# Performance work log

Hardware: AMD Instinct MI355X
Metric: run time of the kernel (lower is better)

Reference implementation:

```python
import jax, jax.numpy as jnp
import numpy as np

S = 64   # state_dim
C = 27   # children per internal node


def setup_inputs() -> dict:
    key = jax.random.key(0)
    ks = jax.random.split(key, 16)
    def f(k, shp, scale=0.02):
        return jax.random.normal(k, shp, dtype=jnp.float32) * scale
    return {
        "external_input": f(ks[0], (S, 5), 1.0),
        "state0":  f(ks[1], (S, 5), 0.01),          # root state buffer
        "states1": f(ks[2], (C, S, 5), 0.01),        # 27 level-1 node states
        "states2": f(ks[3], (C, C, S, 5), 0.01),     # 729 leaf states, grouped by parent
        "agg_W0":  f(ks[4], (S * 5, S * 5 * C)),     # root child_aggregator
        "agg_b0":  f(ks[5], (S * 5,)),
        "agg_W1":  f(ks[6], (C, S * 5, S * 5 * C)),  # batched level-1 aggregators
        "agg_b1":  f(ks[7], (C, S * 5)),
        "up_W1_0": f(ks[8], (64, S * 10)),           # root update_net layer 1
        "up_b1_0": f(ks[9], (64,)),
        "up_W2_0": f(ks[10], (S * 5, 64)),           # root update_net layer 2
        "up_b2_0": f(ks[11], (S * 5,)),
        "up_W1_1": f(ks[12], (C, 64, S * 10)),       # batched level-1 update_nets
        "up_b1_1": f(ks[13], (C, 64)),
        "up_W2_1": f(ks[14], (C, S * 5, 64)),
        "up_b2_1": f(ks[15], (C, S * 5)),
    }


def reference(external_input, state0, states1, states2,
              agg_W0, agg_b0, agg_W1, agg_b1,
              up_W1_0, up_b1_0, up_W2_0, up_b2_0,
              up_W1_1, up_b1_1, up_W2_1, up_b2_1):
    # --- level 2 (leaves): forward just returns their state ---
    leaf_flat = states2.reshape(C, C * S * 5)  # per level-1 parent: stacked+flattened children

    # --- level 1: all 27 nodes processed as one batched GEMV ---
    agg1 = jnp.einsum('nij,nj->ni', agg_W1, leaf_flat) + agg_b1        # [27, S*5]
    comb1 = jnp.concatenate([states1.reshape(C, S * 5), agg1], axis=-1)  # [27, S*10]
    h1 = jax.nn.relu(jnp.einsum('nkj,nj->nk', up_W1_1, comb1) + up_b1_1)  # [27, 64]
    upd1 = jnp.einsum('nij,nj->ni', up_W2_1, h1) + up_b2_1             # [27, S*5]
    new_states1 = states1 + upd1.reshape(C, S, 5)

    # --- root: external input added, then aggregate updated children ---
    s0 = state0 + external_input
    agg0 = agg_W0 @ new_states1.reshape(-1) + agg_b0                   # [S*5]
    comb0 = jnp.concatenate([s0.reshape(-1), agg0])                    # [S*10]
    h0 = jax.nn.relu(up_W1_0 @ comb0 + up_b1_0)
    new_state0 = s0 + (up_W2_0 @ h0 + up_b2_0).reshape(S, 5)
    return new_state0
```

## Files before the change

### kernel.cpp

```cpp
#include <hip/hip_runtime.h>
#include <hip/hip_bf16.h>


__device__ __forceinline__ float wave_reduce_sum(float v) {
    v += __shfl_xor(v, 32, 64);
    v += __shfl_xor(v, 16, 64);
    v += __shfl_xor(v, 8, 64);
    v += __shfl_xor(v, 4, 64);
    v += __shfl_xor(v, 2, 64);
    v += __shfl_xor(v, 1, 64);
    return v;
}

__device__ __forceinline__ float fma4s(float4 w, float4 x, float acc) {
    acc = fmaf(w.x, x.x, acc);
    acc = fmaf(w.y, x.y, acc);
    acc = fmaf(w.z, x.z, acc);
    acc = fmaf(w.w, x.w, acc);
    return acc;
}

__device__ __forceinline__ float4 add4(float4 a, float4 b) {
    return make_float4(a.x + b.x, a.y + b.y, a.z + b.z, a.w + b.w);
}

__global__ void __launch_bounds__(256) k1_gemv(
    const float* __restrict__ W,
    const float* __restrict__ x,
    const float* __restrict__ bias,
    float*       __restrict__ y)
{
    const int b    = blockIdx.x;
    const int node = b / 40;
    const int row0 = node * 320 + (b % 40) * 8;
    const int tid  = threadIdx.x;

    const float4* __restrict__ xf = reinterpret_cast<const float4*>(x) + (size_t)node * 2160;
    const float4* wp[8];
    #pragma unroll
    for (int r = 0; r < 8; ++r)
        wp[r] = reinterpret_cast<const float4*>(W) + (size_t)(row0 + r) * 2160;

    float4 acc[8];
    #pragma unroll
    for (int r = 0; r < 8; ++r) acc[r] = make_float4(0.f, 0.f, 0.f, 0.f);

    for (int j = tid; j < 2160; j += 256) {
        float4 xv = xf[j];
        #pragma unroll
        for (int r = 0; r < 8; ++r) {
            float4 w = wp[r][j];
            acc[r].x = fmaf(w.x, xv.x, acc[r].x);
            acc[r].y = fmaf(w.y, xv.y, acc[r].y);
            acc[r].z = fmaf(w.z, xv.z, acc[r].z);
            acc[r].w = fmaf(w.w, xv.w, acc[r].w);
        }
    }

    float s[8];
    #pragma unroll
    for (int r = 0; r < 8; ++r) {
        s[r] = (acc[r].x + acc[r].y) + (acc[r].z + acc[r].w);
        s[r] = wave_reduce_sum(s[r]);
    }

    __shared__ float red[4][8];
    const int wv = tid >> 6, lane = tid & 63;
    if (lane == 0) {
        #pragma unroll
        for (int r = 0; r < 8; ++r) red[wv][r] = s[r];
    }
    __syncthreads();
    if (tid < 8) {
        float v = red[0][tid] + red[1][tid] + red[2][tid] + red[3][tid];
        y[row0 + tid] = v + bias[row0 + tid];
    }
}

__global__ void __launch_bounds__(256) k2a_h(
    const float* __restrict__ states1,
    const float* __restrict__ agg1,
    const float* __restrict__ W1,
    const float* __restrict__ b1,
    float*       __restrict__ h1)
{
    __shared__ float comb[640];
    const int nb  = blockIdx.x;
    const int n   = nb / 16;
    const int tid = threadIdx.x;

    float4* combf = reinterpret_cast<float4*>(comb);
    const float4* __restrict__ s1f = reinterpret_cast<const float4*>(states1) + (size_t)n * 80;
    const float4* __restrict__ a1f = reinterpret_cast<const float4*>(agg1) + (size_t)n * 80;
    if (tid < 80)       combf[tid] = s1f[tid];
    else if (tid < 160) combf[tid] = a1f[tid - 80];
    __syncthreads();

    const int wv = tid >> 6, lane = tid & 63;
    const int k  = (nb % 16) * 4 + wv;
    const float4* __restrict__ Wf = reinterpret_cast<const float4*>(W1) + ((size_t)n * 64 + k) * 160;
    float acc = 0.f;
    #pragma unroll
    for (int j = lane; j < 160; j += 64)
        acc = fma4s(Wf[j], combf[j], acc);
    acc = wave_reduce_sum(acc);
    if (lane == 0) h1[n * 64 + k] = fmaxf(acc + b1[n * 64 + k], 0.f);
}

__global__ void __launch_bounds__(256) k2b_ns(
    const float* __restrict__ states1,
    const float* __restrict__ h1,
    const float* __restrict__ W2,
    const float* __restrict__ b2,
    float*       __restrict__ ns1)
{
    const int tid  = threadIdx.x;
    const int wv   = tid >> 6, lane = tid & 63;
    const int i    = blockIdx.x * 4 + wv;
    const int n    = i / 320;
    float acc = W2[(size_t)i * 64 + lane] * h1[n * 64 + lane];
    acc = wave_reduce_sum(acc);
    if (lane == 0) ns1[i] = states1[i] + acc + b2[i];
}

__global__ void __launch_bounds__(256) k3_gemv(
    const float* __restrict__ W,
    const float* __restrict__ x,
    float*       __restrict__ yp)
{
    const int b   = blockIdx.x;
    const int cs  = b / 80;
    const int r0  = (b % 80) * 4;
    const int tid = threadIdx.x;

    const float4* __restrict__ xf  = reinterpret_cast<const float4*>(x);
    const float4* __restrict__ w0p = reinterpret_cast<const float4*>(W) + (size_t)(r0 + 0) * 2160;
    const float4* __restrict__ w1p = reinterpret_cast<const float4*>(W) + (size_t)(r0 + 1) * 2160;
    const float4* __restrict__ w2p = reinterpret_cast<const float4*>(W) + (size_t)(r0 + 2) * 2160;
    const float4* __restrict__ w3p = reinterpret_cast<const float4*>(W) + (size_t)(r0 + 3) * 2160;

    float4 a0 = make_float4(0.f, 0.f, 0.f, 0.f), a1 = a0, a2 = a0, a3 = a0;
    const int jend = cs * 540 + 540;
    for (int j = cs * 540 + tid; j < jend; j += 256) {
        float4 xv = xf[j];
        float4 w0 = w0p[j];
        float4 w1 = w1p[j];
        float4 w2 = w2p[j];
        float4 w3 = w3p[j];
        a0.x = fmaf(w0.x, xv.x, a0.x); a0.y = fmaf(w0.y, xv.y, a0.y);
        a0.z = fmaf(w0.z, xv.z, a0.z); a0.w = fmaf(w0.w, xv.w, a0.w);
        a1.x = fmaf(w1.x, xv.x, a1.x); a1.y = fmaf(w1.y, xv.y, a1.y);
        a1.z = fmaf(w1.z, xv.z, a1.z); a1.w = fmaf(w1.w, xv.w, a1.w);
        a2.x = fmaf(w2.x, xv.x, a2.x); a2.y = fmaf(w2.y, xv.y, a2.y);
        a2.z = fmaf(w2.z, xv.z, a2.z); a2.w = fmaf(w2.w, xv.w, a2.w);
        a3.x = fmaf(w3.x, xv.x, a3.x); a3.y = fmaf(w3.y, xv.y, a3.y);
        a3.z = fmaf(w3.z, xv.z, a3.z); a3.w = fmaf(w3.w, xv.w, a3.w);
    }
    float s0 = (a0.x + a0.y) + (a0.z + a0.w);
    float s1 = (a1.x + a1.y) + (a1.z + a1.w);
    float s2 = (a2.x + a2.y) + (a2.z + a2.w);
    float s3 = (a3.x + a3.y) + (a3.z + a3.w);
    s0 = wave_reduce_sum(s0);
    s1 = wave_reduce_sum(s1);
    s2 = wave_reduce_sum(s2);
    s3 = wave_reduce_sum(s3);

    __shared__ float red[4][4];
    const int wv = tid >> 6, lane = tid & 63;
    if (lane == 0) { red[wv][0] = s0; red[wv][1] = s1; red[wv][2] = s2; red[wv][3] = s3; }
    __syncthreads();
    if (tid < 4) {
        yp[cs * 320 + r0 + tid] =
            red[0][tid] + red[1][tid] + red[2][tid] + red[3][tid];
    }
}

__global__ void __launch_bounds__(256) k4a_h(
    const float* __restrict__ state0,
    const float* __restrict__ ext,
    const float* __restrict__ agg0p,
    const float* __restrict__ agg_b0,
    const float* __restrict__ W1,
    const float* __restrict__ b1,
    float*       __restrict__ h0)
{
    __shared__ float comb[640];
    const int tid = threadIdx.x;
    float4* combf = reinterpret_cast<float4*>(comb);
    const float4* __restrict__ s0f = reinterpret_cast<const float4*>(state0);
    const float4* __restrict__ exf = reinterpret_cast<const float4*>(ext);
    const float4* __restrict__ p0  = reinterpret_cast<const float4*>(agg0p);
    const float4* __restrict__ p1  = p0 + 80;
    const float4* __restrict__ p2  = p0 + 160;
    const float4* __restrict__ p3  = p0 + 240;
    const float4* __restrict__ b0f = reinterpret_cast<const float4*>(agg_b0);
    if (tid < 80) {
        combf[tid] = add4(s0f[tid], exf[tid]);
    } else if (tid < 160) {
        int jj = tid - 80;
        combf[tid] = add4(add4(add4(p0[jj], p1[jj]), add4(p2[jj], p3[jj])), b0f[jj]);
    }
    __syncthreads();

    const int wv = tid >> 6, lane = tid & 63;
    const int k  = blockIdx.x * 4 + wv;
    const float4* __restrict__ Wf = reinterpret_cast<const float4*>(W1) + (size_t)k * 160;
    float acc = 0.f;
    #pragma unroll
    for (int j = lane; j < 160; j += 64)
        acc = fma4s(Wf[j], combf[j], acc);
    acc = wave_reduce_sum(acc);
    if (lane == 0) h0[k] = fmaxf(acc + b1[k], 0.f);
}

__global__ void __launch_bounds__(256) k4b_out(
    const float* __restrict__ state0,
    const float* __restrict__ ext,
    const float* __restrict__ h0,
    const float* __restrict__ W2,
    const float* __restrict__ b2,
    float*       __restrict__ out)
{
    const int tid  = threadIdx.x;
    const int wv   = tid >> 6, lane = tid & 63;
    const int i    = blockIdx.x * 4 + wv;
    float acc = W2[(size_t)i * 64 + lane] * h0[lane];
    acc = wave_reduce_sum(acc);
    if (lane == 0) out[i] = state0[i] + ext[i] + acc + b2[i];
}

extern "C" void kernel_launch(void* const* d_in, const int* in_sizes, int n_in,
                              void* d_out, int out_size, void* d_ws, size_t ws_size,
                              hipStream_t stream) {
    const float* ext      = (const float*)d_in[0];
    const float* state0   = (const float*)d_in[1];
    const float* states1  = (const float*)d_in[2];
    const float* states2  = (const float*)d_in[3];
    const float* agg_W0   = (const float*)d_in[4];
    const float* agg_b0   = (const float*)d_in[5];
    const float* agg_W1   = (const float*)d_in[6];
    const float* agg_b1   = (const float*)d_in[7];
    const float* up_W1_0  = (const float*)d_in[8];
    const float* up_b1_0  = (const float*)d_in[9];
    const float* up_W2_0  = (const float*)d_in[10];
    const float* up_b2_0  = (const float*)d_in[11];
    const float* up_W1_1  = (const float*)d_in[12];
    const float* up_b1_1  = (const float*)d_in[13];
    const float* up_W2_1  = (const float*)d_in[14];
    const float* up_b2_1  = (const float*)d_in[15];

    float* out   = (float*)d_out;
    float* ws    = (float*)d_ws;
    float* agg1  = ws;
    float* h1    = ws + 8640;
    float* ns1   = ws + 10368;
    float* agg0p = ws + 19008;
    float* h0    = ws + 20288;

    k1_gemv<<<1080, 256, 0, stream>>>(agg_W1, states2, agg_b1, agg1);
    k2a_h  <<<432,  256, 0, stream>>>(states1, agg1, up_W1_1, up_b1_1, h1);
    k2b_ns <<<2160, 256, 0, stream>>>(states1, h1, up_W2_1, up_b2_1, ns1);
    k3_gemv<<<320,  256, 0, stream>>>(agg_W0, ns1, agg0p);
    k4a_h  <<<16,   256, 0, stream>>>(state0, ext, agg0p, agg_b0, up_W1_0, up_b1_0, h0);
    k4b_out<<<80,   256, 0, stream>>>(state0, ext, h0, up_W2_0, up_b2_0, out);
}
```

Baseline: 71.12 us.

## Fuse per-node update MLP layers into single kernels for level-1 and root

Merges the two-layer update MLP kernels (hidden layer and output layer) into one kernel each for the level-1 nodes and the root, keeping the hidden activations in shared memory. This removes two kernel launches and the global round trips for h1/h0. In exchange, level-1 work now runs on only 27 blocks and the root on a single block, so far fewer CUs pull the roughly 2.2 MB of level-1 update weights.

```diff
diff --git a/kernel.cpp b/kernel.cpp
--- a/kernel.cpp
+++ b/kernel.cpp
@@ -77,17 +77,20 @@
     }
 }
 
-__global__ void __launch_bounds__(256) k2a_h(
+__global__ void __launch_bounds__(512) k2_mlp(
     const float* __restrict__ states1,
     const float* __restrict__ agg1,
     const float* __restrict__ W1,
     const float* __restrict__ b1,
-    float*       __restrict__ h1)
-{
-    __shared__ float comb[640];
-    const int nb  = blockIdx.x;
-    const int n   = nb / 16;
+    const float* __restrict__ W2,
+    const float* __restrict__ b2,
+    float*       __restrict__ ns1)
+{
+    __shared__ __align__(16) float comb[640];
+    __shared__ float h[64];
+    const int n   = blockIdx.x;
     const int tid = threadIdx.x;
+    const int wv  = tid >> 6, lane = tid & 63;
 
     float4* combf = reinterpret_cast<float4*>(comb);
     const float4* __restrict__ s1f = reinterpret_cast<const float4*>(states1) + (size_t)n * 80;
@@ -96,31 +99,33 @@
     else if (tid < 160) combf[tid] = a1f[tid - 80];
     __syncthreads();
 
-    const int wv = tid >> 6, lane = tid & 63;
-    const int k  = (nb % 16) * 4 + wv;
-    const float4* __restrict__ Wf = reinterpret_cast<const float4*>(W1) + ((size_t)n * 64 + k) * 160;
-    float acc = 0.f;
-    #pragma unroll
-    for (int j = lane; j < 160; j += 64)
-        acc = fma4s(Wf[j], combf[j], acc);
-    acc = wave_reduce_sum(acc);
-    if (lane == 0) h1[n * 64 + k] = fmaxf(acc + b1[n * 64 + k], 0.f);
-}
-
-__global__ void __launch_bounds__(256) k2b_ns(
-    const float* __restrict__ states1,
-    const float* __restrict__ h1,
-    const float* __restrict__ W2,
-    const float* __restrict__ b2,
-    float*       __restrict__ ns1)
-{
-    const int tid  = threadIdx.x;
-    const int wv   = tid >> 6, lane = tid & 63;
-    const int i    = blockIdx.x * 4 + wv;
-    const int n    = i / 320;
-    float acc = W2[(size_t)i * 64 + lane] * h1[n * 64 + lane];
-    acc = wave_reduce_sum(acc);
-    if (lane == 0) ns1[i] = states1[i] + acc + b2[i];
+    const float4* __restrict__ cf = reinterpret_cast<const float4*>(comb);
+    #pragma unroll
+    for (int kk = 0; kk < 8; ++kk) {
+        const int k = wv * 8 + kk;
+        const float4* __restrict__ Wf = reinterpret_cast<const float4*>(W1) + ((size_t)n * 64 + k) * 160;
+        float acc = 0.f;
+        #pragma unroll
+        for (int j = lane; j < 160; j += 64)
+            acc = fma4s(Wf[j], cf[j], acc);
+        acc = wave_reduce_sum(acc);
+        if (lane == 0) h[k] = fmaxf(acc + b1[n * 64 + k], 0.f);
+    }
+    __syncthreads();
+
+    if (tid < 320) {
+        const float4* __restrict__ w = reinterpret_cast<const float4*>(W2 + ((size_t)n * 320 + tid) * 64);
+        float acc = 0.f;
+        #pragma unroll
+        for (int j4 = 0; j4 < 16; ++j4) {
+            float4 ww = w[j4];
+            acc = fmaf(ww.x, h[4 * j4 + 0], acc);
+            acc = fmaf(ww.y, h[4 * j4 + 1], acc);
+            acc = fmaf(ww.z, h[4 * j4 + 2], acc);
+            acc = fmaf(ww.w, h[4 * j4 + 3], acc);
+        }
+        ns1[n * 320 + tid] = states1[n * 320 + tid] + acc + b2[n * 320 + tid];
+    }
 }
 
 __global__ void __launch_bounds__(256) k3_gemv(
@@ -175,58 +180,62 @@
     }
 }
 
-__global__ void __launch_bounds__(256) k4a_h(
+__global__ void __launch_bounds__(512) k4_root(
     const float* __restrict__ state0,
     const float* __restrict__ ext,
     const float* __restrict__ agg0p,
-    const float* __restrict__ agg_b0,
+    const float* __restrict__ aggb0,
     const float* __restrict__ W1,
     const float* __restrict__ b1,
-    float*       __restrict__ h0)
-{
-    __shared__ float comb[640];
+    const float* __restrict__ W2,
+    const float* __restrict__ b2,
+    float*       __restrict__ out)
+{
+    __shared__ __align__(16) float comb[640];
+    __shared__ float h[64];
     const int tid = threadIdx.x;
+    const int wv  = tid >> 6, lane = tid & 63;
+
     float4* combf = reinterpret_cast<float4*>(comb);
     const float4* __restrict__ s0f = reinterpret_cast<const float4*>(state0);
     const float4* __restrict__ exf = reinterpret_cast<const float4*>(ext);
     const float4* __restrict__ p0  = reinterpret_cast<const float4*>(agg0p);
-    const float4* __restrict__ p1  = p0 + 80;
-    const float4* __restrict__ p2  = p0 + 160;
-    const float4* __restrict__ p3  = p0 + 240;
-    const float4* __restrict__ b0f = reinterpret_cast<const float4*>(agg_b0);
+    const float4* __restrict__ b0f = reinterpret_cast<const float4*>(aggb0);
     if (tid < 80) {
         combf[tid] = add4(s0f[tid], exf[tid]);
     } else if (tid < 160) {
         int jj = tid - 80;
-        combf[tid] = add4(add4(add4(p0[jj], p1[jj]), add4(p2[jj], p3[jj])), b0f[jj]);
-    }
-    __syncthreads();
-
-    const int wv = tid >> 6, lane = tid & 63;
-    const int k  = blockIdx.x * 4 + wv;
-    const float4* __restrict__ Wf = reinterpret_cast<const float4*>(W1) + (size_t)k * 160;
-    float acc = 0.f;
-    #pragma unroll
-    for (int j = lane; j < 160; j += 64)
-        acc = fma4s(Wf[j], combf[j], acc);
-    acc = wave_reduce_sum(acc);
-    if (lane == 0) h0[k] = fmaxf(acc + b1[k], 0.f);
-}
-
-__global__ void __launch_bounds__(256) k4b_out(
-    const float* __restrict__ state0,
-    const float* __restrict__ ext,
-    const float* __restrict__ h0,
-    const float* __restrict__ W2,
-    const float* __restrict__ b2,
-    float*       __restrict__ out)
-{
-    const int tid  = threadIdx.x;
-    const int wv   = tid >> 6, lane = tid & 63;
-    const int i    = blockIdx.x * 4 + wv;
-    float acc = W2[(size_t)i * 64 + lane] * h0[lane];
-    acc = wave_reduce_sum(acc);
-    if (lane == 0) out[i] = state0[i] + ext[i] + acc + b2[i];
+        combf[tid] = add4(add4(add4(p0[jj], p0[80 + jj]), add4(p0[160 + jj], p0[240 + jj])), b0f[jj]);
+    }
+    __syncthreads();
+
+    const float4* __restrict__ cf = reinterpret_cast<const float4*>(comb);
+    #pragma unroll
+    for (int kk = 0; kk < 8; ++kk) {
+        const int k = wv * 8 + kk;
+        const float4* __restrict__ Wf = reinterpret_cast<const float4*>(W1) + (size_t)k * 160;
+        float acc = 0.f;
+        #pragma unroll
+        for (int j = lane; j < 160; j += 64)
+            acc = fma4s(Wf[j], cf[j], acc);
+        acc = wave_reduce_sum(acc);
+        if (lane == 0) h[k] = fmaxf(acc + b1[k], 0.f);
+    }
+    __syncthreads();
+
+    if (tid < 320) {
+        const float4* __restrict__ w = reinterpret_cast<const float4*>(W2 + (size_t)tid * 64);
+        float acc = 0.f;
+        #pragma unroll
+        for (int j4 = 0; j4 < 16; ++j4) {
+            float4 ww = w[j4];
+            acc = fmaf(ww.x, h[4 * j4 + 0], acc);
+            acc = fmaf(ww.y, h[4 * j4 + 1], acc);
+            acc = fmaf(ww.z, h[4 * j4 + 2], acc);
+            acc = fmaf(ww.w, h[4 * j4 + 3], acc);
+        }
+        out[tid] = comb[tid] + acc + b2[tid];
+    }
 }
 
 extern "C" void kernel_launch(void* const* d_in, const int* in_sizes, int n_in,
@@ -252,15 +261,11 @@
     float* out   = (float*)d_out;
     float* ws    = (float*)d_ws;
     float* agg1  = ws;
-    float* h1    = ws + 8640;
-    float* ns1   = ws + 10368;
-    float* agg0p = ws + 19008;
-    float* h0    = ws + 20288;
+    float* ns1   = ws + 8640;
+    float* agg0p = ws + 17280;
 
     k1_gemv<<<1080, 256, 0, stream>>>(agg_W1, states2, agg_b1, agg1);
-    k2a_h  <<<432,  256, 0, stream>>>(states1, agg1, up_W1_1, up_b1_1, h1);
-    k2b_ns <<<2160, 256, 0, stream>>>(states1, h1, up_W2_1, up_b2_1, ns1);
+    k2_mlp <<<27,   512, 0, stream>>>(states1, agg1, up_W1_1, up_b1_1, up_W2_1, up_b2_1, ns1);
     k3_gemv<<<320,  256, 0, stream>>>(agg_W0, ns1, agg0p);
-    k4a_h  <<<16,   256, 0, stream>>>(state0, ext, agg0p, agg_b0, up_W1_0, up_b1_0, h0);
-    k4b_out<<<80,   256, 0, stream>>>(state0, ext, h0, up_W2_0, up_b2_0, out);
-}
+    k4_root<<<1,    512, 0, stream>>>(state0, ext, agg0p, agg_b0, up_W1_0, up_b1_0, up_W2_0, up_b2_0, out);
+}
```

New measurement: 95.55 us. +34.4%, slower.
